# Performance work log

Measured on AMD Instinct MI355X. Metric: run time of the kernel, lower is better.

The kernel has to match this reference:

```python
import jax, jax.numpy as jnp
import numpy as np

HEADS = 8
EPS = 1e-5


def layernorm(x, g, b):
    mu = jnp.mean(x, axis=-1, keepdims=True)
    var = jnp.mean((x - mu) ** 2, axis=-1, keepdims=True)
    return (x - mu) * jax.lax.rsqrt(var + EPS) * g + b


def setup_inputs() -> dict:
    key = jax.random.key(0)
    ks = jax.random.split(key, 5)
    B, C, H, W = 8, 384, 32, 32
    d = C
    s = 0.02
    return {
        "x": jax.random.normal(ks[0], (B, C, H, W), jnp.float32),
        "ln1_g": jnp.ones((d,), jnp.float32),
        "ln1_b": jnp.zeros((d,), jnp.float32),
        "lna_g": jnp.ones((d,), jnp.float32),
        "lna_b": jnp.zeros((d,), jnp.float32),
        "w_qkv": jax.random.normal(ks[1], (d, 3 * d), jnp.float32) * s,
        "w_out": jax.random.normal(ks[2], (d, d), jnp.float32) * s,
        "ln2_g": jnp.ones((d,), jnp.float32),
        "ln2_b": jnp.zeros((d,), jnp.float32),
        "w1": jax.random.normal(ks[3], (d, 4 * d), jnp.float32) * s,
        "b1": jnp.zeros((4 * d,), jnp.float32),
        "w2": jax.random.normal(ks[4], (4 * d, d), jnp.float32) * s,
        "b2": jnp.zeros((d,), jnp.float32),
    }


def reference(x, ln1_g, ln1_b, lna_g, lna_b, w_qkv, w_out, ln2_g, ln2_b, w1, b1, w2, b2):
    B, C, H, W = x.shape
    d = C
    dh = d // HEADS
    scale = dh ** (-0.5)
    # flatten spatial -> tokens: [B, N, C]
    t = x.reshape(B, C, H * W).transpose(0, 2, 1)

    # --- attention branch (note: double pre-norm, as in original) ---
    a = layernorm(t, ln1_g, ln1_b)
    a = layernorm(a, lna_g, lna_b)
    qkv = a @ w_qkv  # [B, N, 3d]
    q, k, v = jnp.split(qkv, 3, axis=-1)
    q = q.reshape(B, -1, HEADS, dh).transpose(0, 2, 1, 3)  # b h n d
    k = k.reshape(B, -1, HEADS, dh).transpose(0, 2, 1, 3)
    v = v.reshape(B, -1, HEADS, dh).transpose(0, 2, 1, 3)
    dots = jnp.einsum("bhnd,bhmd->bhnm", q, k) * scale
    attn = jax.nn.softmax(dots, axis=-1)
    o = jnp.einsum("bhnm,bhmd->bhnd", attn, v)
    o = o.transpose(0, 2, 1, 3).reshape(B, -1, d)
    t = t + o @ w_out

    # --- MLP branch (exact GELU, as torch nn.GELU default) ---
    m = layernorm(t, ln2_g, ln2_b)
    m = jax.nn.gelu(m @ w1 + b1, approximate=False) @ w2 + b2
    t = t + m

    return t.transpose(0, 2, 1).reshape(B, C, H, W)
```

## Files before the change

kernel.cpp:

```cpp
#include <hip/hip_runtime.h>
#include <math.h>

#define NTOK 1024
#define DM   384
#define NHEAD 8
#define DH   48
#define BATCH 8
#define NROWS (BATCH * NTOK)
#define SCALE 0.14433756729740643f

typedef __attribute__((ext_vector_type(8))) short bf16x8;
typedef __attribute__((ext_vector_type(4))) float f32x4;

#define ASYNC16(gp, lp) __builtin_amdgcn_global_load_lds( \
    (const __attribute__((address_space(1))) void*)(gp),  \
    (__attribute__((address_space(3))) void*)(lp), 16, 0, 0)

__device__ __forceinline__ unsigned short f2bf(float f) {
    unsigned int u = __float_as_uint(f);
    u += 0x7fffu + ((u >> 16) & 1u);
    return (unsigned short)(u >> 16);
}

__device__ __forceinline__ float gelu_exact(float v) {
    return 0.5f * v * (1.0f + erff(v * 0.70710678118654752f));
}

__global__ __launch_bounds__(256) void transpose_kernel(const float* __restrict__ src,
                                                        float* __restrict__ dst,
                                                        int rows, int cols) {
    __shared__ float tile[32][33];
    const size_t sb = (size_t)blockIdx.z * rows * cols;
    const int r0 = blockIdx.y * 32, c0 = blockIdx.x * 32;
    const int tx = threadIdx.x & 31, ty = threadIdx.x >> 5;
    #pragma unroll
    for (int i = ty; i < 32; i += 8)
        tile[i][tx] = src[sb + (size_t)(r0 + i) * cols + (c0 + tx)];
    __syncthreads();
    #pragma unroll
    for (int i = ty; i < 32; i += 8)
        dst[sb + (size_t)(c0 + i) * rows + (r0 + tx)] = tile[tx][i];
}

__global__ __launch_bounds__(256) void wprep_all(const float* __restrict__ wqkv,
                                                 const float* __restrict__ wout,
                                                 const float* __restrict__ w1,
                                                 const float* __restrict__ w2,
                                                 unsigned short* __restrict__ wqkvT,
                                                 unsigned short* __restrict__ woutT,
                                                 unsigned short* __restrict__ w1T,
                                                 unsigned short* __restrict__ w2T) {
    __shared__ float tile[32][33];
    const int bid = blockIdx.x;
    const float* W; unsigned short* Wt; int K, N, nx, t;
    if (bid < 432)       { W = wqkv; Wt = wqkvT; K = 384;  N = 1152; nx = 36; t = bid; }
    else if (bid < 576)  { W = wout; Wt = woutT; K = 384;  N = 384;  nx = 12; t = bid - 432; }
    else if (bid < 1152) { W = w1;   Wt = w1T;   K = 384;  N = 1536; nx = 48; t = bid - 576; }
    else                 { W = w2;   Wt = w2T;   K = 1536; N = 384;  nx = 12; t = bid - 1152; }
    const int n0 = (t % nx) * 32, k0 = (t / nx) * 32;
    const int tx = threadIdx.x & 31, ty = threadIdx.x >> 5;
    #pragma unroll
    for (int i = ty; i < 32; i += 8)
        tile[i][tx] = W[(size_t)(k0 + i) * N + n0 + tx];
    __syncthreads();
    #pragma unroll
    for (int i = ty; i < 32; i += 8)
        Wt[(size_t)(n0 + i) * K + k0 + tx] = f2bf(tile[tx][i]);
}

template <bool DOUBLE>
__global__ __launch_bounds__(384) void ln_kernel(const float* __restrict__ in,
                                                 const float* __restrict__ g1,
                                                 const float* __restrict__ b1,
                                                 const float* __restrict__ g2,
                                                 const float* __restrict__ b2,
                                                 unsigned short* __restrict__ outp) {
    const int row = blockIdx.x;
    const int c = threadIdx.x;
    __shared__ float rs[6], rq[6];
    float v = in[(size_t)row * DM + c];

    float s = v, sq = v * v;
    #pragma unroll
    for (int off = 32; off; off >>= 1) {
        s += __shfl_xor(s, off, 64);
        sq += __shfl_xor(sq, off, 64);
    }
    const int wid = c >> 6;
    if ((c & 63) == 0) { rs[wid] = s; rq[wid] = sq; }
    __syncthreads();
    s = rs[0] + rs[1] + rs[2] + rs[3] + rs[4] + rs[5];
    sq = rq[0] + rq[1] + rq[2] + rq[3] + rq[4] + rq[5];
    float mu = s * (1.0f / DM);
    float var = fmaxf(sq * (1.0f / DM) - mu * mu, 0.0f);
    float y = (v - mu) * rsqrtf(var + 1e-5f) * g1[c] + b1[c];

    if (DOUBLE) {
        __syncthreads();
        s = y; sq = y * y;
        #pragma unroll
        for (int off = 32; off; off >>= 1) {
            s += __shfl_xor(s, off, 64);
            sq += __shfl_xor(sq, off, 64);
        }
        if ((c & 63) == 0) { rs[wid] = s; rq[wid] = sq; }
        __syncthreads();
        s = rs[0] + rs[1] + rs[2] + rs[3] + rs[4] + rs[5];
        sq = rq[0] + rq[1] + rq[2] + rq[3] + rq[4] + rq[5];
        mu = s * (1.0f / DM);
        var = fmaxf(sq * (1.0f / DM) - mu * mu, 0.0f);
        y = (y - mu) * rsqrtf(var + 1e-5f) * g2[c] + b2[c];
    }
    outp[(size_t)row * DM + c] = f2bf(y);
}

template <int EPI>
__global__ __launch_bounds__(256) void gemm_bf16(const unsigned short* __restrict__ A,
                                                 const unsigned short* __restrict__ Bt,
                                                 const float* __restrict__ bias,
                                                 const float* __restrict__ R,
                                                 unsigned short* __restrict__ Cbf,
                                                 float* __restrict__ Cf,
                                                 int M, int N, int K) {
    __shared__ unsigned short As[128][64];
    __shared__ unsigned short Bs[128][64];
    const int tid = threadIdx.x;
    const int w = tid >> 6, lane = tid & 63;
    const int l15 = lane & 15, lq = lane >> 4;
    const int bm = blockIdx.y * 128, bn = blockIdx.x * 128;
    const int moff = (w & 1) * 64, noff = (w >> 1) * 64;

    const int srw = lane >> 3, pp = lane & 7;
    const int c = pp ^ srw;
    const unsigned short* Ag[4];
    const unsigned short* Bg[4];
    #pragma unroll
    for (int j = 0; j < 4; ++j) {
        const int row = w * 32 + j * 8 + srw;
        Ag[j] = A + (size_t)(bm + row) * K + c * 8;
        Bg[j] = Bt + (size_t)(bn + row) * K + c * 8;
    }

    const int octA = ((lq ^ (l15 & 7)) << 4);

    f32x4 acc[4][4];
    #pragma unroll
    for (int mi = 0; mi < 4; ++mi)
        #pragma unroll
        for (int ni = 0; ni < 4; ++ni) acc[mi][ni] = (f32x4){0.f, 0.f, 0.f, 0.f};

    for (int k0 = 0; k0 < K; k0 += 64) {
        __syncthreads();
        #pragma unroll
        for (int j = 0; j < 4; ++j) {
            ASYNC16(Ag[j], &As[w * 32 + j * 8][0]);
            ASYNC16(Bg[j], &Bs[w * 32 + j * 8][0]);
            Ag[j] += 64; Bg[j] += 64;
        }
        __syncthreads();
        #pragma unroll
        for (int ks = 0; ks < 2; ++ks) {
            const int ox = octA ^ (ks << 6);
            bf16x8 af[4], bfr[4];
            #pragma unroll
            for (int mi = 0; mi < 4; ++mi)
                af[mi] = *(const bf16x8*)((const char*)As + ((moff + mi * 16 + l15) << 7) + ox);
            #pragma unroll
            for (int ni = 0; ni < 4; ++ni)
                bfr[ni] = *(const bf16x8*)((const char*)Bs + ((noff + ni * 16 + l15) << 7) + ox);
            #pragma unroll
            for (int mi = 0; mi < 4; ++mi)
                #pragma unroll
                for (int ni = 0; ni < 4; ++ni)
                    acc[mi][ni] = __builtin_amdgcn_mfma_f32_16x16x32_bf16(af[mi], bfr[ni], acc[mi][ni], 0, 0, 0);
        }
    }

    #pragma unroll
    for (int mi = 0; mi < 4; ++mi) {
        #pragma unroll
        for (int ni = 0; ni < 4; ++ni) {
            const int col = bn + noff + ni * 16 + l15;
            float bv = 0.0f;
            if (EPI >= 2) bv = bias[col];
            #pragma unroll
            for (int r = 0; r < 4; ++r) {
                const int row = bm + moff + mi * 16 + lq * 4 + r;
                const size_t idx = (size_t)row * N + col;
                float v = acc[mi][ni][r];
                if (EPI == 2) v = gelu_exact(v + bv);
                if (EPI == 3) v += bv;
                if (EPI == 0 || EPI == 2) Cbf[idx] = f2bf(v);
                else                      Cf[idx] = v + R[idx];
            }
        }
    }
}

__global__ __launch_bounds__(256) void attn_kernel(const unsigned short* __restrict__ qkv,
                                                   unsigned short* __restrict__ o) {
    __shared__ unsigned short Qs[64][64];
    __shared__ unsigned short Ks[64][64];
    __shared__ unsigned short Vt[48][72];
    __shared__ unsigned short Pm[64][88];
    __shared__ float Lred[4][64];

    const int tid = threadIdx.x;
    const int w = tid >> 6, lane = tid & 63;
    const int l15 = lane & 15, lq = lane >> 4;
    const int bid = blockIdx.x;
    const int xm = bid >> 3;
    const int bh = ((xm & 7) << 3) | (bid & 7);
    const int qt0 = (xm >> 3) * 64;
    const int h = bh & 7, b = bh >> 3;

    const unsigned short* qbase = qkv + (size_t)b * NTOK * 1152 + h * 48;
    const unsigned short* kbase = qbase + 384;
    const unsigned short* vbase = qbase + 768;

    #pragma unroll
    for (int s0 = 0; s0 < 2; ++s0) {
        const int s = tid + s0 * 256;
        const int row = s >> 3, p = s & 7;
        const int cc = p ^ (row & 7);
        uint4 val = make_uint4(0, 0, 0, 0);
        if (cc < 6) val = *(const uint4*)(qbase + (size_t)(qt0 + row) * 1152 + cc * 8);
        *(uint4*)((char*)Qs + row * 128 + p * 16) = val;
    }

    const int srw = lane >> 3, pp = lane & 7;
    const int ck = pp ^ srw;
    const int ckoff = (ck < 6) ? ck * 8 : (ck - 6) * 8;
    const unsigned short* Kg0 = kbase + (size_t)(w * 16 + srw) * 1152 + ckoff;
    const unsigned short* Kg1 = Kg0 + 8 * 1152;

    const int vtp = tid & 31, vfo = tid >> 5;
    const unsigned short* Vg = vbase + (size_t)(vtp * 2) * 1152 + vfo * 8;

    const int octK = ((lq ^ (l15 & 7)) << 4);

    f32x4 oacc[3];
    float lpart[4] = {0.f, 0.f, 0.f, 0.f};
    #pragma unroll
    for (int mi = 0; mi < 3; ++mi) oacc[mi] = (f32x4){0.f, 0.f, 0.f, 0.f};

    for (int kt = 0; kt < 16; ++kt) {
        __syncthreads();
        ASYNC16(Kg0, &Ks[w * 16][0]);
        ASYNC16(Kg1, &Ks[w * 16 + 8][0]);
        Kg0 += 64 * 1152; Kg1 += 64 * 1152;
        if (vfo < 6) {
            const uint4 va = *(const uint4*)Vg;
            const uint4 vb = *(const uint4*)(Vg + 1152);
            const unsigned short* ashort = (const unsigned short*)&va;
            const unsigned short* bshort = (const unsigned short*)&vb;
            #pragma unroll
            for (int j = 0; j < 8; ++j) {
                const unsigned int dw = (unsigned int)ashort[j] | ((unsigned int)bshort[j] << 16);
                *(unsigned int*)((char*)Vt + (vfo * 8 + j) * 144 + vtp * 4) = dw;
            }
        }
        Vg += 64 * 1152;
        __syncthreads();

        f32x4 sacc[4];
        #pragma unroll
        for (int ni = 0; ni < 4; ++ni) sacc[ni] = (f32x4){0.f, 0.f, 0.f, 0.f};
        #pragma unroll
        for (int ks = 0; ks < 2; ++ks) {
            const int ox = octK ^ (ks << 6);
            const bf16x8 kf = *(const bf16x8*)((const char*)Ks + ((w * 16 + l15) << 7) + ox);
            #pragma unroll
            for (int ni = 0; ni < 4; ++ni) {
                const bf16x8 qf = *(const bf16x8*)((const char*)Qs + ((ni * 16 + l15) << 7) + ox);
                sacc[ni] = __builtin_amdgcn_mfma_f32_16x16x32_bf16(kf, qf, sacc[ni], 0, 0, 0);
            }
        }

        #pragma unroll
        for (int ni = 0; ni < 4; ++ni) {
            const float p0 = __expf(sacc[ni][0] * SCALE);
            const float p1 = __expf(sacc[ni][1] * SCALE);
            const float p2 = __expf(sacc[ni][2] * SCALE);
            const float p3 = __expf(sacc[ni][3] * SCALE);
            lpart[ni] += (p0 + p1) + (p2 + p3);
            uint2 d;
            d.x = (unsigned int)f2bf(p0) | ((unsigned int)f2bf(p1) << 16);
            d.y = (unsigned int)f2bf(p2) | ((unsigned int)f2bf(p3) << 16);
            *(uint2*)((char*)Pm + (ni * 16 + l15) * 176 + (w * 16 + lq * 4) * 2) = d;
        }
        __syncthreads();

        #pragma unroll
        for (int ks = 0; ks < 2; ++ks) {
            const int kk2 = (ks * 32 + lq * 8) * 2;
            const bf16x8 pf = *(const bf16x8*)((const char*)Pm + (w * 16 + l15) * 176 + kk2);
            #pragma unroll
            for (int mi = 0; mi < 3; ++mi) {
                const bf16x8 vf = *(const bf16x8*)((const char*)Vt + (mi * 16 + l15) * 144 + kk2);
                oacc[mi] = __builtin_amdgcn_mfma_f32_16x16x32_bf16(vf, pf, oacc[mi], 0, 0, 0);
            }
        }
    }

    #pragma unroll
    for (int ni = 0; ni < 4; ++ni) {
        float ls = lpart[ni];
        ls += __shfl_xor(ls, 16, 64);
        ls += __shfl_xor(ls, 32, 64);
        if (lq == 0) Lred[w][ni * 16 + l15] = ls;
    }
    __syncthreads();
    const int myq = w * 16 + l15;
    const float linv = 1.0f / (Lred[0][myq] + Lred[1][myq] + Lred[2][myq] + Lred[3][myq]);

    unsigned short* ob = o + (size_t)(b * NTOK + qt0 + myq) * DM + h * DH;
    #pragma unroll
    for (int mi = 0; mi < 3; ++mi) {
        uint2 d;
        d.x = (unsigned int)f2bf(oacc[mi][0] * linv) | ((unsigned int)f2bf(oacc[mi][1] * linv) << 16);
        d.y = (unsigned int)f2bf(oacc[mi][2] * linv) | ((unsigned int)f2bf(oacc[mi][3] * linv) << 16);
        *(uint2*)(ob + mi * 16 + lq * 4) = d;
    }
}

extern "C" void kernel_launch(void* const* d_in, const int* in_sizes, int n_in,
                              void* d_out, int out_size, void* d_ws, size_t ws_size,
                              hipStream_t stream) {
    const float* x     = (const float*)d_in[0];
    const float* ln1_g = (const float*)d_in[1];
    const float* ln1_b = (const float*)d_in[2];
    const float* lna_g = (const float*)d_in[3];
    const float* lna_b = (const float*)d_in[4];
    const float* w_qkv = (const float*)d_in[5];
    const float* w_out = (const float*)d_in[6];
    const float* ln2_g = (const float*)d_in[7];
    const float* ln2_b = (const float*)d_in[8];
    const float* w1    = (const float*)d_in[9];
    const float* b1    = (const float*)d_in[10];
    const float* w2    = (const float*)d_in[11];
    const float* b2    = (const float*)d_in[12];
    float* out = (float*)d_out;

    char* wsb = (char*)d_ws;
    float* t               = (float*)(wsb);
    unsigned short* a_bf   = (unsigned short*)(wsb + 12582912);
    unsigned short* qkv_bf = (unsigned short*)(wsb + 18874368);
    unsigned short* o_bf   = (unsigned short*)(wsb + 37748736);
    unsigned short* h1_bf  = (unsigned short*)(wsb + 44040192);
    unsigned short* wqkvT  = (unsigned short*)(wsb + 69206016);
    unsigned short* woutT  = (unsigned short*)(wsb + 70090752);
    unsigned short* w1T    = (unsigned short*)(wsb + 70385664);
    unsigned short* w2T    = (unsigned short*)(wsb + 71565312);

    wprep_all<<<1728, 256, 0, stream>>>(w_qkv, w_out, w1, w2, wqkvT, woutT, w1T, w2T);
    transpose_kernel<<<dim3(32, 12, 8), 256, 0, stream>>>(x, t, DM, NTOK);
    ln_kernel<true><<<NROWS, DM, 0, stream>>>(t, ln1_g, ln1_b, lna_g, lna_b, a_bf);
    gemm_bf16<0><<<dim3(9, 64), 256, 0, stream>>>(a_bf, wqkvT, nullptr, nullptr, qkv_bf, nullptr, NROWS, 3 * DM, DM);
    attn_kernel<<<1024, 256, 0, stream>>>(qkv_bf, o_bf);
    gemm_bf16<1><<<dim3(3, 64), 256, 0, stream>>>(o_bf, woutT, nullptr, t, nullptr, t, NROWS, DM, DM);
    ln_kernel<false><<<NROWS, DM, 0, stream>>>(t, ln2_g, ln2_b, nullptr, nullptr, a_bf);
    gemm_bf16<2><<<dim3(12, 64), 256, 0, stream>>>(a_bf, w1T, b1, nullptr, h1_bf, nullptr, NROWS, 4 * DM, DM);
    gemm_bf16<3><<<dim3(3, 64), 256, 0, stream>>>(h1_bf, w2T, b2, t, nullptr, t, NROWS, DM, 4 * DM);
    transpose_kernel<<<dim3(12, 32, 8), 256, 0, stream>>>(t, out, NTOK, DM);
}
```

Baseline: 253.3 us.

## Switch to fp16 operands and give each wave its own query rows in attention

Replaces bf16 with fp16 for weights, activations and MFMA ops throughout, using hardware packed conversion (cvt_pkrtz) instead of the software bf16 rounding. In attention, each wave now owns 16 query rows and loops over all key blocks, writing P into a per-wave buffer. This removes a block-wide barrier per tile and the cross-wave row-sum reduction at the end. exp2f with a prescaled constant replaces expf. fp16 has a narrower range, and the softmax is computed without max subtraction, which could overflow for large logits.

```diff
diff --git a/kernel.cpp b/kernel.cpp
--- a/kernel.cpp
+++ b/kernel.cpp
@@ -8,18 +8,20 @@
 #define BATCH 8
 #define NROWS (BATCH * NTOK)
 #define SCALE 0.14433756729740643f
-
-typedef __attribute__((ext_vector_type(8))) short bf16x8;
+#define SC2   (0.14433756729740643f * 1.4426950408889634f)
+
+typedef __attribute__((ext_vector_type(8))) _Float16 f16x8;
+typedef __attribute__((ext_vector_type(2))) __fp16 fp16x2_raw;
 typedef __attribute__((ext_vector_type(4))) float f32x4;
 
 #define ASYNC16(gp, lp) __builtin_amdgcn_global_load_lds( \
     (const __attribute__((address_space(1))) void*)(gp),  \
     (__attribute__((address_space(3))) void*)(lp), 16, 0, 0)
 
-__device__ __forceinline__ unsigned short f2bf(float f) {
-    unsigned int u = __float_as_uint(f);
-    u += 0x7fffu + ((u >> 16) & 1u);
-    return (unsigned short)(u >> 16);
+__device__ __forceinline__ unsigned int pkh(float a, float b) {
+    union { fp16x2_raw h; unsigned int u; } cv;
+    cv.h = __builtin_amdgcn_cvt_pkrtz(a, b);
+    return cv.u;
 }
 
 __device__ __forceinline__ float gelu_exact(float v) {
@@ -46,13 +48,13 @@
                                                  const float* __restrict__ wout,
                                                  const float* __restrict__ w1,
                                                  const float* __restrict__ w2,
-                                                 unsigned short* __restrict__ wqkvT,
-                                                 unsigned short* __restrict__ woutT,
-                                                 unsigned short* __restrict__ w1T,
-                                                 unsigned short* __restrict__ w2T) {
+                                                 _Float16* __restrict__ wqkvT,
+                                                 _Float16* __restrict__ woutT,
+                                                 _Float16* __restrict__ w1T,
+                                                 _Float16* __restrict__ w2T) {
     __shared__ float tile[32][33];
     const int bid = blockIdx.x;
-    const float* W; unsigned short* Wt; int K, N, nx, t;
+    const float* W; _Float16* Wt; int K, N, nx, t;
     if (bid < 432)       { W = wqkv; Wt = wqkvT; K = 384;  N = 1152; nx = 36; t = bid; }
     else if (bid < 576)  { W = wout; Wt = woutT; K = 384;  N = 384;  nx = 12; t = bid - 432; }
     else if (bid < 1152) { W = w1;   Wt = w1T;   K = 384;  N = 1536; nx = 48; t = bid - 576; }
@@ -65,7 +67,7 @@
     __syncthreads();
     #pragma unroll
     for (int i = ty; i < 32; i += 8)
-        Wt[(size_t)(n0 + i) * K + k0 + tx] = f2bf(tile[tx][i]);
+        Wt[(size_t)(n0 + i) * K + k0 + tx] = (_Float16)tile[tx][i];
 }
 
 template <bool DOUBLE>
@@ -74,7 +76,7 @@
                                                  const float* __restrict__ b1,
                                                  const float* __restrict__ g2,
                                                  const float* __restrict__ b2,
-                                                 unsigned short* __restrict__ outp) {
+                                                 _Float16* __restrict__ outp) {
     const int row = blockIdx.x;
     const int c = threadIdx.x;
     __shared__ float rs[6], rq[6];
@@ -111,19 +113,19 @@
         var = fmaxf(sq * (1.0f / DM) - mu * mu, 0.0f);
         y = (y - mu) * rsqrtf(var + 1e-5f) * g2[c] + b2[c];
     }
-    outp[(size_t)row * DM + c] = f2bf(y);
+    outp[(size_t)row * DM + c] = (_Float16)y;
 }
 
 template <int EPI>
-__global__ __launch_bounds__(256) void gemm_bf16(const unsigned short* __restrict__ A,
-                                                 const unsigned short* __restrict__ Bt,
-                                                 const float* __restrict__ bias,
-                                                 const float* __restrict__ R,
-                                                 unsigned short* __restrict__ Cbf,
-                                                 float* __restrict__ Cf,
-                                                 int M, int N, int K) {
-    __shared__ unsigned short As[128][64];
-    __shared__ unsigned short Bs[128][64];
+__global__ __launch_bounds__(256) void gemm_f16(const _Float16* __restrict__ A,
+                                                const _Float16* __restrict__ Bt,
+                                                const float* __restrict__ bias,
+                                                const float* __restrict__ R,
+                                                _Float16* __restrict__ Ch,
+                                                float* __restrict__ Cf,
+                                                int M, int N, int K) {
+    __shared__ _Float16 As[128][64];
+    __shared__ _Float16 Bs[128][64];
     const int tid = threadIdx.x;
     const int w = tid >> 6, lane = tid & 63;
     const int l15 = lane & 15, lq = lane >> 4;
@@ -132,8 +134,8 @@
 
     const int srw = lane >> 3, pp = lane & 7;
     const int c = pp ^ srw;
-    const unsigned short* Ag[4];
-    const unsigned short* Bg[4];
+    const _Float16* Ag[4];
+    const _Float16* Bg[4];
     #pragma unroll
     for (int j = 0; j < 4; ++j) {
         const int row = w * 32 + j * 8 + srw;
@@ -161,18 +163,18 @@
         #pragma unroll
         for (int ks = 0; ks < 2; ++ks) {
             const int ox = octA ^ (ks << 6);
-            bf16x8 af[4], bfr[4];
+            f16x8 af[4], bfr[4];
             #pragma unroll
             for (int mi = 0; mi < 4; ++mi)
-                af[mi] = *(const bf16x8*)((const char*)As + ((moff + mi * 16 + l15) << 7) + ox);
+                af[mi] = *(const f16x8*)((const char*)As + ((moff + mi * 16 + l15) << 7) + ox);
             #pragma unroll
             for (int ni = 0; ni < 4; ++ni)
-                bfr[ni] = *(const bf16x8*)((const char*)Bs + ((noff + ni * 16 + l15) << 7) + ox);
+                bfr[ni] = *(const f16x8*)((const char*)Bs + ((noff + ni * 16 + l15) << 7) + ox);
             #pragma unroll
             for (int mi = 0; mi < 4; ++mi)
                 #pragma unroll
                 for (int ni = 0; ni < 4; ++ni)
-                    acc[mi][ni] = __builtin_amdgcn_mfma_f32_16x16x32_bf16(af[mi], bfr[ni], acc[mi][ni], 0, 0, 0);
+                    acc[mi][ni] = __builtin_amdgcn_mfma_f32_16x16x32_f16(af[mi], bfr[ni], acc[mi][ni], 0, 0, 0);
         }
     }
 
@@ -190,20 +192,19 @@
                 float v = acc[mi][ni][r];
                 if (EPI == 2) v = gelu_exact(v + bv);
                 if (EPI == 3) v += bv;
-                if (EPI == 0 || EPI == 2) Cbf[idx] = f2bf(v);
+                if (EPI == 0 || EPI == 2) Ch[idx] = (_Float16)v;
                 else                      Cf[idx] = v + R[idx];
             }
         }
     }
 }
 
-__global__ __launch_bounds__(256) void attn_kernel(const unsigned short* __restrict__ qkv,
-                                                   unsigned short* __restrict__ o) {
-    __shared__ unsigned short Qs[64][64];
-    __shared__ unsigned short Ks[64][64];
-    __shared__ unsigned short Vt[48][72];
-    __shared__ unsigned short Pm[64][88];
-    __shared__ float Lred[4][64];
+__global__ __launch_bounds__(256) void attn_kernel(const _Float16* __restrict__ qkv,
+                                                   _Float16* __restrict__ o) {
+    __shared__ _Float16 Qs[64][64];
+    __shared__ _Float16 Ks[64][64];
+    __shared__ _Float16 Vt[48][72];
+    __shared__ _Float16 Ps[4][16][72];
 
     const int tid = threadIdx.x;
     const int w = tid >> 6, lane = tid & 63;
@@ -214,9 +215,9 @@
     const int qt0 = (xm >> 3) * 64;
     const int h = bh & 7, b = bh >> 3;
 
-    const unsigned short* qbase = qkv + (size_t)b * NTOK * 1152 + h * 48;
-    const unsigned short* kbase = qbase + 384;
-    const unsigned short* vbase = qbase + 768;
+    const _Float16* qbase = qkv + (size_t)b * NTOK * 1152 + h * 48;
+    const _Float16* kbase = qbase + 384;
+    const _Float16* vbase = qbase + 768;
 
     #pragma unroll
     for (int s0 = 0; s0 < 2; ++s0) {
@@ -231,16 +232,16 @@
     const int srw = lane >> 3, pp = lane & 7;
     const int ck = pp ^ srw;
     const int ckoff = (ck < 6) ? ck * 8 : (ck - 6) * 8;
-    const unsigned short* Kg0 = kbase + (size_t)(w * 16 + srw) * 1152 + ckoff;
-    const unsigned short* Kg1 = Kg0 + 8 * 1152;
+    const _Float16* Kg0 = kbase + (size_t)(w * 16 + srw) * 1152 + ckoff;
+    const _Float16* Kg1 = Kg0 + 8 * 1152;
 
     const int vtp = tid & 31, vfo = tid >> 5;
-    const unsigned short* Vg = vbase + (size_t)(vtp * 2) * 1152 + vfo * 8;
+    const _Float16* Vg = vbase + (size_t)(vtp * 2) * 1152 + vfo * 8;
 
     const int octK = ((lq ^ (l15 & 7)) << 4);
 
     f32x4 oacc[3];
-    float lpart[4] = {0.f, 0.f, 0.f, 0.f};
+    float lpart = 0.0f;
     #pragma unroll
     for (int mi = 0; mi < 3; ++mi) oacc[mi] = (f32x4){0.f, 0.f, 0.f, 0.f};
 
@@ -265,61 +266,53 @@
 
         f32x4 sacc[4];
         #pragma unroll
-        for (int ni = 0; ni < 4; ++ni) sacc[ni] = (f32x4){0.f, 0.f, 0.f, 0.f};
+        for (int mi = 0; mi < 4; ++mi) sacc[mi] = (f32x4){0.f, 0.f, 0.f, 0.f};
         #pragma unroll
         for (int ks = 0; ks < 2; ++ks) {
             const int ox = octK ^ (ks << 6);
-            const bf16x8 kf = *(const bf16x8*)((const char*)Ks + ((w * 16 + l15) << 7) + ox);
-            #pragma unroll
-            for (int ni = 0; ni < 4; ++ni) {
-                const bf16x8 qf = *(const bf16x8*)((const char*)Qs + ((ni * 16 + l15) << 7) + ox);
-                sacc[ni] = __builtin_amdgcn_mfma_f32_16x16x32_bf16(kf, qf, sacc[ni], 0, 0, 0);
+            const f16x8 qf = *(const f16x8*)((const char*)Qs + ((w * 16 + l15) << 7) + ox);
+            #pragma unroll
+            for (int mi = 0; mi < 4; ++mi) {
+                const f16x8 kf = *(const f16x8*)((const char*)Ks + ((mi * 16 + l15) << 7) + ox);
+                sacc[mi] = __builtin_amdgcn_mfma_f32_16x16x32_f16(kf, qf, sacc[mi], 0, 0, 0);
             }
         }
 
         #pragma unroll
-        for (int ni = 0; ni < 4; ++ni) {
-            const float p0 = __expf(sacc[ni][0] * SCALE);
-            const float p1 = __expf(sacc[ni][1] * SCALE);
-            const float p2 = __expf(sacc[ni][2] * SCALE);
-            const float p3 = __expf(sacc[ni][3] * SCALE);
-            lpart[ni] += (p0 + p1) + (p2 + p3);
+        for (int mi = 0; mi < 4; ++mi) {
+            const float p0 = exp2f(sacc[mi][0] * SC2);
+            const float p1 = exp2f(sacc[mi][1] * SC2);
+            const float p2 = exp2f(sacc[mi][2] * SC2);
+            const float p3 = exp2f(sacc[mi][3] * SC2);
+            lpart += (p0 + p1) + (p2 + p3);
             uint2 d;
-            d.x = (unsigned int)f2bf(p0) | ((unsigned int)f2bf(p1) << 16);
-            d.y = (unsigned int)f2bf(p2) | ((unsigned int)f2bf(p3) << 16);
-            *(uint2*)((char*)Pm + (ni * 16 + l15) * 176 + (w * 16 + lq * 4) * 2) = d;
-        }
-        __syncthreads();
+            d.x = pkh(p0, p1); d.y = pkh(p2, p3);
+            *(uint2*)&Ps[w][l15][mi * 16 + lq * 4] = d;
+        }
+        asm volatile("s_waitcnt lgkmcnt(0)" ::: "memory");
 
         #pragma unroll
         for (int ks = 0; ks < 2; ++ks) {
             const int kk2 = (ks * 32 + lq * 8) * 2;
-            const bf16x8 pf = *(const bf16x8*)((const char*)Pm + (w * 16 + l15) * 176 + kk2);
+            const f16x8 pf = *(const f16x8*)&Ps[w][l15][ks * 32 + lq * 8];
             #pragma unroll
             for (int mi = 0; mi < 3; ++mi) {
-                const bf16x8 vf = *(const bf16x8*)((const char*)Vt + (mi * 16 + l15) * 144 + kk2);
-                oacc[mi] = __builtin_amdgcn_mfma_f32_16x16x32_bf16(vf, pf, oacc[mi], 0, 0, 0);
+                const f16x8 vf = *(const f16x8*)((const char*)Vt + (mi * 16 + l15) * 144 + kk2);
+                oacc[mi] = __builtin_amdgcn_mfma_f32_16x16x32_f16(vf, pf, oacc[mi], 0, 0, 0);
             }
         }
     }
 
-    #pragma unroll
-    for (int ni = 0; ni < 4; ++ni) {
-        float ls = lpart[ni];
-        ls += __shfl_xor(ls, 16, 64);
-        ls += __shfl_xor(ls, 32, 64);
-        if (lq == 0) Lred[w][ni * 16 + l15] = ls;
-    }
-    __syncthreads();
-    const int myq = w * 16 + l15;
-    const float linv = 1.0f / (Lred[0][myq] + Lred[1][myq] + Lred[2][myq] + Lred[3][myq]);
-
-    unsigned short* ob = o + (size_t)(b * NTOK + qt0 + myq) * DM + h * DH;
+    lpart += __shfl_xor(lpart, 16, 64);
+    lpart += __shfl_xor(lpart, 32, 64);
+    const float linv = 1.0f / lpart;
+
+    _Float16* ob = o + (size_t)(b * NTOK + qt0 + w * 16 + l15) * DM + h * DH;
     #pragma unroll
     for (int mi = 0; mi < 3; ++mi) {
         uint2 d;
-        d.x = (unsigned int)f2bf(oacc[mi][0] * linv) | ((unsigned int)f2bf(oacc[mi][1] * linv) << 16);
-        d.y = (unsigned int)f2bf(oacc[mi][2] * linv) | ((unsigned int)f2bf(oacc[mi][3] * linv) << 16);
+        d.x = pkh(oacc[mi][0] * linv, oacc[mi][1] * linv);
+        d.y = pkh(oacc[mi][2] * linv, oacc[mi][3] * linv);
         *(uint2*)(ob + mi * 16 + lq * 4) = d;
     }
 }
@@ -343,24 +336,24 @@
     float* out = (float*)d_out;
 
     char* wsb = (char*)d_ws;
-    float* t               = (float*)(wsb);
-    unsigned short* a_bf   = (unsigned short*)(wsb + 12582912);
-    unsigned short* qkv_bf = (unsigned short*)(wsb + 18874368);
-    unsigned short* o_bf   = (unsigned short*)(wsb + 37748736);
-    unsigned short* h1_bf  = (unsigned short*)(wsb + 44040192);
-    unsigned short* wqkvT  = (unsigned short*)(wsb + 69206016);
-    unsigned short* woutT  = (unsigned short*)(wsb + 70090752);
-    unsigned short* w1T    = (unsigned short*)(wsb + 70385664);
-    unsigned short* w2T    = (unsigned short*)(wsb + 71565312);
+    float* t          = (float*)(wsb);
+    _Float16* a_h     = (_Float16*)(wsb + 12582912);
+    _Float16* qkv_h   = (_Float16*)(wsb + 18874368);
+    _Float16* o_h     = (_Float16*)(wsb + 37748736);
+    _Float16* h1_h    = (_Float16*)(wsb + 44040192);
+    _Float16* wqkvT   = (_Float16*)(wsb + 69206016);
+    _Float16* woutT   = (_Float16*)(wsb + 70090752);
+    _Float16* w1T     = (_Float16*)(wsb + 70385664);
+    _Float16* w2T     = (_Float16*)(wsb + 71565312);
 
     wprep_all<<<1728, 256, 0, stream>>>(w_qkv, w_out, w1, w2, wqkvT, woutT, w1T, w2T);
     transpose_kernel<<<dim3(32, 12, 8), 256, 0, stream>>>(x, t, DM, NTOK);
-    ln_kernel<true><<<NROWS, DM, 0, stream>>>(t, ln1_g, ln1_b, lna_g, lna_b, a_bf);
-    gemm_bf16<0><<<dim3(9, 64), 256, 0, stream>>>(a_bf, wqkvT, nullptr, nullptr, qkv_bf, nullptr, NROWS, 3 * DM, DM);
-    attn_kernel<<<1024, 256, 0, stream>>>(qkv_bf, o_bf);
-    gemm_bf16<1><<<dim3(3, 64), 256, 0, stream>>>(o_bf, woutT, nullptr, t, nullptr, t, NROWS, DM, DM);
-    ln_kernel<false><<<NROWS, DM, 0, stream>>>(t, ln2_g, ln2_b, nullptr, nullptr, a_bf);
-    gemm_bf16<2><<<dim3(12, 64), 256, 0, stream>>>(a_bf, w1T, b1, nullptr, h1_bf, nullptr, NROWS, 4 * DM, DM);
-    gemm_bf16<3><<<dim3(3, 64), 256, 0, stream>>>(h1_bf, w2T, b2, t, nullptr, t, NROWS, DM, 4 * DM);
+    ln_kernel<true><<<NROWS, DM, 0, stream>>>(t, ln1_g, ln1_b, lna_g, lna_b, a_h);
+    gemm_f16<0><<<dim3(9, 64), 256, 0, stream>>>(a_h, wqkvT, nullptr, nullptr, qkv_h, nullptr, NROWS, 3 * DM, DM);
+    attn_kernel<<<1024, 256, 0, stream>>>(qkv_h, o_h);
+    gemm_f16<1><<<dim3(3, 64), 256, 0, stream>>>(o_h, woutT, nullptr, t, nullptr, t, NROWS, DM, DM);
+    ln_kernel<false><<<NROWS, DM, 0, stream>>>(t, ln2_g, ln2_b, nullptr, nullptr, a_h);
+    gemm_f16<2><<<dim3(12, 64), 256, 0, stream>>>(a_h, w1T, b1, nullptr, h1_h, nullptr, NROWS, 4 * DM, DM);
+    gemm_f16<3><<<dim3(3, 64), 256, 0, stream>>>(h1_h, w2T, b2, t, nullptr, t, NROWS, DM, 4 * DM);
     transpose_kernel<<<dim3(12, 32, 8), 256, 0, stream>>>(t, out, NTOK, DM);
 }
```

After: 267.8 us. +5.7%, slower.
